# Optimization experiments

Measured on AMD Instinct MI355X. Metric: run time of the kernel, lower is better.

## Reference

```python
import jax, jax.numpy as jnp
import numpy as np

B, T, M, S, D, H, DH, P = 4, 1024, 1024, 1024, 1024, 16, 64, 4096


def layernorm(x, g, b, eps=1e-5):
    mu = x.mean(-1, keepdims=True)
    var = ((x - mu) ** 2).mean(-1, keepdims=True)
    return (x - mu) * jax.lax.rsqrt(var + eps) * g + b


def rel_shift(x):
    # Transformer-XL relative shift on [B,H,q,k] BD scores
    b, h, q, k = x.shape
    x = jnp.pad(x, ((0, 0), (0, 0), (0, 0), (1, 0)))
    return x.reshape(b, h, k + 1, q)[:, :, 1:, :].reshape(b, h, q, k)


def rel_attention(x, kv, mem, mask, pos_emb, r_w_bias, r_r_bias,
                  Wq, Wk, Wv, Wr, Wo, g, bln):
    # x: [B,Tq,D] queries; kv: [B,Skv,D]; mem: optional [B,M,D]
    cat = kv if mem is None else jnp.concatenate([mem, kv], axis=1)
    Bb, Tq, _ = x.shape
    K = cat.shape[1]
    q = (x @ Wq).reshape(Bb, Tq, H, DH)
    k = (cat @ Wk).reshape(Bb, K, H, DH)
    v = (cat @ Wv).reshape(Bb, K, H, DH)
    r = (pos_emb[-K:] @ Wr).reshape(K, H, DH)  # rel-pos keys, most-recent K positions
    AC = jnp.einsum('bthd,bkhd->bhtk', q + r_w_bias, k)
    BD = rel_shift(jnp.einsum('bthd,khd->bhtk', q + r_r_bias, r))
    scores = (AC + BD) * (1.0 / np.sqrt(DH))
    scores = jnp.where(mask[:, None, :, :], jnp.asarray(-1e30, scores.dtype), scores)
    prob = jax.nn.softmax(scores, axis=-1)
    o = jnp.einsum('bhtk,bkhd->bthd', prob, v).reshape(Bb, Tq, H * DH) @ Wo
    return layernorm(x + o, g, bln), cat, prob  # post-LN residual; cat is new memory


def residual_ff(x, W1, b1, W2, b2, g, bln):
    h = jax.nn.relu(x @ W1 + b1) @ W2 + b2
    return layernorm(x + h, g, bln)


def setup_inputs() -> dict:
    key = jax.random.key(0)
    ks = jax.random.split(key, 24)
    w = lambda i, shape: jax.random.normal(ks[i], shape, jnp.float32) * 0.02
    causal = jnp.triu(jnp.ones((T, M + T), bool), k=M + 1)  # True = masked
    return {
        'src': jax.random.normal(ks[0], (B, S, D), jnp.float32),
        'tgt': jax.random.normal(ks[1], (B, T, D), jnp.float32),
        'tgt_mem': jax.random.normal(ks[2], (B, M, D), jnp.float32),
        'pos_emb': w(3, (M + T, D)),
        'r_w_bias': w(4, (H, DH)),
        'r_r_bias': w(5, (H, DH)),
        'Wq1': w(6, (D, H * DH)), 'Wk1': w(7, (D, H * DH)), 'Wv1': w(8, (D, H * DH)),
        'Wr1': w(9, (D, H * DH)), 'Wo1': w(10, (H * DH, D)),
        'ln1_g': jnp.ones((D,), jnp.float32), 'ln1_b': jnp.zeros((D,), jnp.float32),
        'Wq2': w(11, (D, H * DH)), 'Wk2': w(12, (D, H * DH)), 'Wv2': w(13, (D, H * DH)),
        'Wr2': w(14, (D, H * DH)), 'Wo2': w(15, (H * DH, D)),
        'ln2_g': jnp.ones((D,), jnp.float32), 'ln2_b': jnp.zeros((D,), jnp.float32),
        'Wf1': w(16, (D, P)), 'bf1': jnp.zeros((P,), jnp.float32),
        'Wf2': w(17, (P, D)), 'bf2': jnp.zeros((D,), jnp.float32),
        'ln3_g': jnp.ones((D,), jnp.float32), 'ln3_b': jnp.zeros((D,), jnp.float32),
        'tgt_mask': jnp.broadcast_to(causal, (B, T, M + T)),
        'tgt_to_src_mask': jnp.zeros((B, T, S), bool),
    }


def reference(src, tgt, tgt_mem, pos_emb, r_w_bias, r_r_bias,
              Wq1, Wk1, Wv1, Wr1, Wo1, ln1_g, ln1_b,
              Wq2, Wk2, Wv2, Wr2, Wo2, ln2_g, ln2_b,
              Wf1, bf1, Wf2, bf2, ln3_g, ln3_b,
              tgt_mask, tgt_to_src_mask):
    out, new_mem, self_att_prob = rel_attention(
        tgt, tgt, tgt_mem, tgt_mask, pos_emb, r_w_bias, r_r_bias,
        Wq1, Wk1, Wv1, Wr1, Wo1, ln1_g, ln1_b)
    out, _, inter_att_prob = rel_attention(
        out, src, None, tgt_to_src_mask, pos_emb, r_w_bias, r_r_bias,
        Wq2, Wk2, Wv2, Wr2, Wo2, ln2_g, ln2_b)
    out = residual_ff(out, Wf1, bf1, Wf2, bf2, ln3_g, ln3_b)
    return (out, new_mem, self_att_prob, inter_att_prob)
```

## Files before the change

kernel.cpp:

```cpp
#include <hip/hip_runtime.h>

typedef unsigned short u16;
typedef __attribute__((ext_vector_type(8))) short short8;
typedef __attribute__((ext_vector_type(4))) float f4;
typedef __attribute__((ext_vector_type(4))) unsigned short u16x4;

__device__ __forceinline__ float b2f(u16 u) {
    unsigned int x = ((unsigned int)u) << 16;
    return __builtin_bit_cast(float, x);
}
__device__ __forceinline__ u16 f2b(float f) {
    unsigned int u = __builtin_bit_cast(unsigned int, f);
    u += 0x7FFFu + ((u >> 16) & 1u);
    return (u16)(u >> 16);
}

__device__ __forceinline__ void gl16(const void* g, void* l) {
    __builtin_amdgcn_global_load_lds(
        (const __attribute__((address_space(1))) void*)g,
        (__attribute__((address_space(3))) void*)l, 16, 0, 0);
}

template<int FM, int FN, int CBF, int EPI>
__global__ __launch_bounds__(256, 3)
void gemm_bt(const u16* __restrict__ Ap, const u16* __restrict__ Bp,
             void* __restrict__ Cp, const float* __restrict__ bias,
             int M, int N, int K, int lda, int ldb, int ldc,
             long long sAh, long long sAb, long long sBh, long long sBb,
             long long sCh, long long sCb, int batchH)
{
    constexpr int BM = FM * 32;
    constexpr int BN = FN * 32;
    __shared__ __align__(16) u16 As[2][BM * 32];
    __shared__ __align__(16) u16 Bs[2][BN * 32];

    const int tid  = threadIdx.x;
    const int z    = blockIdx.z;
    const int bb   = z / batchH;
    const int hh   = z - bb * batchH;
    const int m0   = blockIdx.y * BM;
    const int n0   = blockIdx.x * BN;
    const int w    = tid >> 6;
    const int lane = tid & 63;
    const int wr   = w >> 1;
    const int wc   = w & 1;
    const int lrow = lane & 15;
    const int lk   = (lane >> 4) << 3;
    const int lrow4 = lane >> 2;
    const int lch   = lane & 3;

    const u16* Ag = Ap + sAb * bb + sAh * hh;
    const u16* Bg = Bp + sBb * bb + sBh * hh;

    f4 acc[FM][FN] = {};

    auto stage = [&](int buf, int kt) {
        const int kb = kt << 5;
        #pragma unroll
        for (int i = 0; i < BM / 64; ++i) {
            const int row0 = (w + i * 4) << 4;
            gl16(Ag + (long long)(m0 + row0 + lrow4) * lda + kb + (lch << 3),
                 &As[buf][row0 * 32]);
        }
        #pragma unroll
        for (int i = 0; i < BN / 64; ++i) {
            const int row0 = (w + i * 4) << 4;
            gl16(Bg + (long long)(n0 + row0 + lrow4) * ldb + kb + (lch << 3),
                 &Bs[buf][row0 * 32]);
        }
    };

    const int nKt = K >> 5;
    stage(0, 0);
    __syncthreads();
    int cur = 0;
    for (int kt = 0; kt < nKt; ++kt) {
        if (kt + 1 < nKt) stage(cur ^ 1, kt + 1);

        short8 af[FM], bv[FN];
        #pragma unroll
        for (int m = 0; m < FM; ++m)
            af[m] = *(const short8*)(&As[cur][(wr * FM * 16 + m * 16 + lrow) * 32 + lk]);
        #pragma unroll
        for (int n = 0; n < FN; ++n)
            bv[n] = *(const short8*)(&Bs[cur][(wc * FN * 16 + n * 16 + lrow) * 32 + lk]);
        #pragma unroll
        for (int m = 0; m < FM; ++m)
            #pragma unroll
            for (int n = 0; n < FN; ++n)
                acc[m][n] = __builtin_amdgcn_mfma_f32_16x16x32_bf16(af[m], bv[n], acc[m][n], 0, 0, 0);

        __syncthreads();
        cur ^= 1;
    }

    const int crow0 = m0 + wr * FM * 16 + ((lane >> 4) << 2);
    const int ccol0 = n0 + wc * FN * 16 + lrow;
    if (CBF == 0) {
        float* Cg = (float*)Cp + sCb * bb + sCh * hh;
        #pragma unroll
        for (int m = 0; m < FM; ++m) {
            #pragma unroll
            for (int n = 0; n < FN; ++n) {
                const int col = ccol0 + n * 16;
                float bvv = (EPI >= 1) ? bias[col] : 0.f;
                #pragma unroll
                for (int r = 0; r < 4; ++r) {
                    float vv = acc[m][n][r] + bvv;
                    if (EPI == 2) vv = fmaxf(vv, 0.f);
                    Cg[(long long)(crow0 + m * 16 + r) * ldc + col] = vv;
                }
            }
        }
    } else {
        u16* Cg = (u16*)Cp + sCb * bb + sCh * hh;
        #pragma unroll
        for (int m = 0; m < FM; ++m) {
            #pragma unroll
            for (int n = 0; n < FN; ++n) {
                const int col = ccol0 + n * 16;
                float bvv = (EPI >= 1) ? bias[col] : 0.f;
                #pragma unroll
                for (int r = 0; r < 4; ++r) {
                    float vv = acc[m][n][r] + bvv;
                    if (EPI == 2) vv = fmaxf(vv, 0.f);
                    Cg[(long long)(crow0 + m * 16 + r) * ldc + col] = f2b(vv);
                }
            }
        }
    }
}

template<int KK, int MODE>
__global__ __launch_bounds__(512, 4)
void fattn(const u16* __restrict__ qsrc, long long qld, long long qsb,
           const float* __restrict__ rwb, const float* __restrict__ rrb,
           const u16* __restrict__ kb, const u16* __restrict__ rr,
           const u16* __restrict__ vt,
           float* __restrict__ probs, u16* __restrict__ ob, int kld)
{
    constexpr int LE = KK + 8;
    constexpr int NT = KK / 16;
    constexpr int NI = NT / 8;
    __shared__ __align__(16) u16 e[16 * LE];
    __shared__ __align__(16) u16 qws[16 * 72];
    __shared__ __align__(16) u16 qrs[17 * 72];
    __shared__ float psum[8][16];

    const int tid = threadIdx.x;
    const int bh  = blockIdx.y;
    const int b   = bh >> 4, h = bh & 15;
    const int t0  = blockIdx.x << 4;

    if (tid < 264) {
        int row, ch; const float* bias; u16* dst; bool act = true;
        if (tid < 128)      { row = tid >> 3;        ch = tid & 7; bias = rwb; dst = &qws[row * 72 + ch * 8]; }
        else if (tid < 256) { row = (tid - 128) >> 3; ch = tid & 7; bias = rrb; dst = &qrs[row * 72 + ch * 8]; }
        else if (MODE == 1) { row = 16;              ch = tid - 256; bias = rrb; dst = &qrs[16 * 72 + ch * 8]; }
        else act = false;
        if (act) {
            int trow = t0 + row; if (trow > 1023) trow = 1023;
            short8 qv = *(const short8*)(qsrc + b * qsb + (long long)trow * qld + h * 64 + ch * 8);
            const float* bp = bias + h * 64 + ch * 8;
            f4 b0 = *(const f4*)bp, b1 = *(const f4*)(bp + 4);
            short8 o;
            o[0] = (short)f2b((b2f((u16)qv[0]) + b0.x) * 0.125f);
            o[1] = (short)f2b((b2f((u16)qv[1]) + b0.y) * 0.125f);
            o[2] = (short)f2b((b2f((u16)qv[2]) + b0.z) * 0.125f);
            o[3] = (short)f2b((b2f((u16)qv[3]) + b0.w) * 0.125f);
            o[4] = (short)f2b((b2f((u16)qv[4]) + b1.x) * 0.125f);
            o[5] = (short)f2b((b2f((u16)qv[5]) + b1.y) * 0.125f);
            o[6] = (short)f2b((b2f((u16)qv[6]) + b1.z) * 0.125f);
            o[7] = (short)f2b((b2f((u16)qv[7]) + b1.w) * 0.125f);
            *(short8*)dst = o;
        }
    }
    __syncthreads();

    const int w = tid >> 6, lane = tid & 63;
    const int lc = lane & 15, g = lane >> 4, lk = g << 3;
    const int t = t0 + lc;

    const short8 bq0 = *(const short8*)&qws[lc * 72 + lk];
    const short8 bq1 = *(const short8*)&qws[lc * 72 + 32 + lk];
    const short8 br0 = *(const short8*)&qrs[lc * 72 + lk];
    const short8 br1 = *(const short8*)&qrs[lc * 72 + 32 + lk];
    short8 bs0 = {}, bs1 = {};
    if (MODE == 1) {
        bs0 = *(const short8*)&qrs[(lc + 1) * 72 + lk];
        bs1 = *(const short8*)&qrs[(lc + 1) * 72 + 32 + lk];
    }

    #pragma unroll
    for (int Bb = 0; Bb < NI; Bb += 2) {
        short8 R0[2], R1[2];
        #pragma unroll
        for (int u = 0; u < 2; ++u) {
            const int ut = w + (Bb + u) * 8;
            const int u0 = ut << 4;
            const bool nd = (u0 + t0 + 30 >= 1023) || (MODE == 1 && u0 + t0 <= 1021);
            if (nd) {
                const u16* rg = rr + (long long)(u0 + lc) * 2048 + h * 64;
                R0[u] = *(const short8*)(rg + lk);
                R1[u] = *(const short8*)(rg + 32 + lk);
            }
        }
        #pragma unroll
        for (int u = 0; u < 2; ++u) {
            const int ut = w + (Bb + u) * 8;
            const int u0 = ut << 4;
            const bool need1 = (u0 + t0 + 30 >= 1023);
            const bool need2 = (MODE == 1) && (u0 + t0 <= 1021);
            if (need1) {
                f4 acc = {};
                acc = __builtin_amdgcn_mfma_f32_16x16x32_bf16(R0[u], br0, acc, 0, 0, 0);
                acc = __builtin_amdgcn_mfma_f32_16x16x32_bf16(R1[u], br1, acc, 0, 0, 0);
                #pragma unroll
                for (int i = 0; i < 4; ++i) {
                    const int j = u0 + 4 * g + i + t - 1023;
                    if (j >= 0) e[lc * LE + j] = f2b(acc[i]);
                }
            }
            if (MODE == 1 && need2) {
                f4 acc = {};
                acc = __builtin_amdgcn_mfma_f32_16x16x32_bf16(R0[u], bs0, acc, 0, 0, 0);
                acc = __builtin_amdgcn_mfma_f32_16x16x32_bf16(R1[u], bs1, acc, 0, 0, 0);
                #pragma unroll
                for (int i = 0; i < 4; ++i) {
                    const int j = u0 + 4 * g + i + t + 2;
                    if (j < KK) e[lc * LE + j] = f2b(acc[i]);
                }
            }
        }
    }
    __syncthreads();

    float sum = 0.f;
    const int limit = t + 1024;
    const int jvt = (MODE == 0) ? ((t0 + 1039) >> 4) : (NT - 1);
    #pragma unroll
    for (int Bb = 0; Bb < NI; Bb += 4) {
        short8 K0[4], K1[4];
        #pragma unroll
        for (int u = 0; u < 4; ++u) {
            const int jt = w + (Bb + u) * 8;
            if (MODE != 0 || jt <= jvt) {
                const u16* kg = kb + (long long)(b * KK + (jt << 4) + lc) * kld + h * 64;
                K0[u] = *(const short8*)(kg + lk);
                K1[u] = *(const short8*)(kg + 32 + lk);
            }
        }
        #pragma unroll
        for (int u = 0; u < 4; ++u) {
            const int jt = w + (Bb + u) * 8;
            const int jme = (jt << 4) + 4 * g;
            if (MODE == 0 && jt > jvt) {
                u16x4 z = {0, 0, 0, 0};
                *(u16x4*)&e[lc * LE + jme] = z;
            } else {
                f4 acc = {};
                acc = __builtin_amdgcn_mfma_f32_16x16x32_bf16(K0[u], bq0, acc, 0, 0, 0);
                acc = __builtin_amdgcn_mfma_f32_16x16x32_bf16(K1[u], bq1, acc, 0, 0, 0);
                u16x4 bd4 = *(const u16x4*)&e[lc * LE + jme];
                u16x4 st;
                #pragma unroll
                for (int i = 0; i < 4; ++i) {
                    const int j = jme + i;
                    float bd = b2f(bd4[i]);
                    if (MODE == 1 && j == t + 1) bd = 0.f;
                    float ev = __expf(acc[i] + bd);
                    if (MODE == 0 && j > limit) ev = 0.f;
                    sum += ev;
                    st[i] = f2b(ev);
                }
                *(u16x4*)&e[lc * LE + jme] = st;
            }
        }
    }
    sum += __shfl_xor(sum, 16);
    sum += __shfl_xor(sum, 32);
    if (g == 0) psum[w][lc] = sum;
    __syncthreads();

    if (w >= 4) {
        const int r = (tid >> 4) & 15;
        const int q = tid & 15;
        float s = 0.f;
        #pragma unroll
        for (int w2 = 0; w2 < 8; ++w2) s += psum[w2][r];
        const float inv = 1.f / s;
        float* pr = probs + ((long long)bh * 1024 + t0 + r) * KK;
        #pragma unroll 4
        for (int i2 = 0; i2 < KK / 128; ++i2) {
            const int j0 = q * 8 + i2 * 128;
            u16x4 e0 = *(const u16x4*)&e[r * LE + j0];
            u16x4 e1 = *(const u16x4*)&e[r * LE + j0 + 4];
            f4 p0, p1;
            p0.x = b2f(e0.x) * inv; p0.y = b2f(e0.y) * inv;
            p0.z = b2f(e0.z) * inv; p0.w = b2f(e0.w) * inv;
            p1.x = b2f(e1.x) * inv; p1.y = b2f(e1.y) * inv;
            p1.z = b2f(e1.z) * inv; p1.w = b2f(e1.w) * inv;
            __builtin_nontemporal_store(p0, (f4*)(pr + j0));
            __builtin_nontemporal_store(p1, (f4*)(pr + j0 + 4));
        }
    } else {
        const int db = w << 4;
        const u16* vrow = vt + ((long long)(bh * 64 + db + lc)) * KK + lk;
        int kcend = KK / 32;
        if (MODE == 0) {
            const int ke = (t0 + 1071) >> 5;
            if (ke < kcend) kcend = ke;
        }
        f4 acc = {};
        #pragma unroll 2
        for (int kc = 0; kc < kcend; ++kc) {
            short8 a = *(const short8*)&e[lc * LE + kc * 32 + lk];
            short8 bv = *(const short8*)(vrow + kc * 32);
            acc = __builtin_amdgcn_mfma_f32_16x16x32_bf16(a, bv, acc, 0, 0, 0);
        }
        #pragma unroll
        for (int i = 0; i < 4; ++i) {
            const int trow = g * 4 + i;
            float s = 0.f;
            #pragma unroll
            for (int w2 = 0; w2 < 8; ++w2) s += psum[w2][trow];
            ob[((long long)(b * 1024 + t0 + trow)) * 1024 + h * 64 + db + lc] = f2b(acc[i] / s);
        }
    }
}

__global__ void conv_f2b(const float* __restrict__ in, u16* __restrict__ out, long long n4)
{
    long long i = (long long)blockIdx.x * 256 + threadIdx.x;
    if (i >= n4) return;
    f4 v = *(const f4*)(in + i * 4);
    u16x4 o; o.x = f2b(v.x); o.y = f2b(v.y); o.z = f2b(v.z); o.w = f2b(v.w);
    *(u16x4*)(out + i * 4) = o;
}

__global__ void concat_mem(const float* __restrict__ mem, const float* __restrict__ tgt,
                           float* __restrict__ nm, u16* __restrict__ cat)
{
    long long i = (long long)blockIdx.x * 256 + threadIdx.x;
    long long b = i >> 19;
    int rem = (int)(i & 524287);
    int r = rem >> 8, c4 = rem & 255;
    const float* sp = (r < 1024) ? (mem + ((b << 10) + r) * 1024 + c4 * 4)
                                 : (tgt + ((b << 10) + (r - 1024)) * 1024 + c4 * 4);
    f4 v = *(const f4*)sp;
    __builtin_nontemporal_store(v, (f4*)(nm + i * 4));
    u16x4 o; o.x = f2b(v.x); o.y = f2b(v.y); o.z = f2b(v.z); o.w = f2b(v.w);
    *(u16x4*)(cat + i * 4) = o;
}

struct TWS { const float* s; u16* d; int sld, dld; };
struct TW18 { TWS t[18]; };
__global__ void transpose_w18(TW18 p)
{
    __shared__ float tile[32][33];
    const TWS ts = p.t[blockIdx.z];
    int c0 = blockIdx.x * 32, r0 = blockIdx.y * 32;
    int tx = threadIdx.x, ty = threadIdx.y;
    tile[ty][tx] = ts.s[(long long)(r0 + ty) * ts.sld + c0 + tx];
    __syncthreads();
    ts.d[(long long)(c0 + ty) * ts.dld + r0 + tx] = f2b(tile[tx][ty]);
}

__global__ __launch_bounds__(256) void transpose_v(const u16* __restrict__ v, u16* __restrict__ vt,
                                                   int KK, int ld, int coff)
{
    __shared__ u16 tile[64][68];
    const int z = blockIdx.z, b = z >> 4, h = z & 15;
    const int j0 = blockIdx.x << 6;
    const int rr8 = threadIdx.x >> 3;
    const int c8 = (threadIdx.x & 7) << 3;
    #pragma unroll
    for (int p = 0; p < 2; ++p) {
        const int jr = p * 32 + rr8;
        short8 val = *(const short8*)(v + ((long long)(b * KK + j0 + jr)) * ld + coff + h * 64 + c8);
        #pragma unroll
        for (int k = 0; k < 8; ++k) tile[c8 + k][jr] = (u16)val[k];
    }
    __syncthreads();
    #pragma unroll
    for (int p = 0; p < 2; ++p) {
        const int d = p * 32 + rr8;
        short8 o;
        #pragma unroll
        for (int k = 0; k < 8; ++k) o[k] = (short)tile[d][c8 + k];
        *(short8*)(vt + ((long long)((b * 16 + h) * 64 + d)) * KK + j0 + c8) = o;
    }
}

__global__ __launch_bounds__(256) void ln_res(const float* __restrict__ x,
                                              const float* __restrict__ h1,
                                              const float* __restrict__ h2,
                                              const float* __restrict__ hbias,
                                              const float* __restrict__ g, const float* __restrict__ bl,
                                              float* __restrict__ o32, u16* __restrict__ obf)
{
    const long long row = blockIdx.x;
    const int tid = threadIdx.x;
    const long long base = row * 1024 + tid * 4;
    f4 xa = *(const f4*)(x + base);
    f4 ha = *(const f4*)(h1 + base);
    f4 hb = *(const f4*)(h2 + base);
    f4 hc = {0.f, 0.f, 0.f, 0.f};
    if (hbias) hc = *(const f4*)(hbias + tid * 4);
    float v0 = xa.x + ha.x + hb.x + hc.x, v1 = xa.y + ha.y + hb.y + hc.y;
    float v2 = xa.z + ha.z + hb.z + hc.z, v3 = xa.w + ha.w + hb.w + hc.w;
    float lsum = v0 + v1 + v2 + v3;
    float lsq = v0 * v0 + v1 * v1 + v2 * v2 + v3 * v3;
    #pragma unroll
    for (int o2 = 32; o2; o2 >>= 1) { lsum += __shfl_xor(lsum, o2); lsq += __shfl_xor(lsq, o2); }
    __shared__ float r1[4], r2[4];
    int w = tid >> 6, lane = tid & 63;
    if (lane == 0) { r1[w] = lsum; r2[w] = lsq; }
    __syncthreads();
    lsum = r1[0] + r1[1] + r1[2] + r1[3];
    lsq  = r2[0] + r2[1] + r2[2] + r2[3];
    const float mu = lsum * 0.0009765625f;
    const float var = lsq * 0.0009765625f - mu * mu;
    const float rsd = rsqrtf(var + 1e-5f);
    const int c = tid * 4;
    f4 gv = *(const f4*)(g + c);
    f4 bv = *(const f4*)(bl + c);
    f4 y;
    y.x = (v0 - mu) * rsd * gv.x + bv.x;
    y.y = (v1 - mu) * rsd * gv.y + bv.y;
    y.z = (v2 - mu) * rsd * gv.z + bv.z;
    y.w = (v3 - mu) * rsd * gv.w + bv.w;
    *(f4*)(o32 + base) = y;
    if (obf) {
        u16x4 u; u.x = f2b(y.x); u.y = f2b(y.y); u.z = f2b(y.z); u.w = f2b(y.w);
        *(u16x4*)(obf + base) = u;
    }
}

extern "C" void kernel_launch(void* const* d_in, const int* in_sizes, int n_in,
                              void* d_out, int out_size, void* d_ws, size_t ws_size,
                              hipStream_t stream)
{
    (void)in_sizes; (void)n_in; (void)out_size;
    const float* src  = (const float*)d_in[0];
    const float* tgt  = (const float*)d_in[1];
    const float* mem  = (const float*)d_in[2];
    const float* pos  = (const float*)d_in[3];
    const float* rwb  = (const float*)d_in[4];
    const float* rrb  = (const float*)d_in[5];
    const float* Wq1  = (const float*)d_in[6];
    const float* Wk1  = (const float*)d_in[7];
    const float* Wv1  = (const float*)d_in[8];
    const float* Wr1  = (const float*)d_in[9];
    const float* Wo1  = (const float*)d_in[10];
    const float* ln1g = (const float*)d_in[11];
    const float* ln1b = (const float*)d_in[12];
    const float* Wq2  = (const float*)d_in[13];
    const float* Wk2  = (const float*)d_in[14];
    const float* Wv2  = (const float*)d_in[15];
    const float* Wr2  = (const float*)d_in[16];
    const float* Wo2  = (const float*)d_in[17];
    const float* ln2g = (const float*)d_in[18];
    const float* ln2b = (const float*)d_in[19];
    const float* Wf1  = (const float*)d_in[20];
    const float* bf1  = (const float*)d_in[21];
    const float* Wf2  = (const float*)d_in[22];
    const float* bf2  = (const float*)d_in[23];
    const float* ln3g = (const float*)d_in[24];
    const float* ln3b = (const float*)d_in[25];

    float* outp   = (float*)d_out;
    float* newmem = outp + 4194304;
    float* selfP  = outp + 12582912;
    float* interP = outp + 146800640;

    char* ws = (char*)d_ws;
    size_t off = 0;
    auto alloc = [&](size_t bytes) -> void* {
        void* p = ws + off;
        off = (off + bytes + 255) & ~(size_t)255;
        return p;
    };
    u16*   src_bf  = (u16*)alloc(8u << 20);
    u16*   cat_bf  = (u16*)alloc(16u << 20);
    u16*   pos_bf  = (u16*)alloc(4u << 20);
    u16*   W1t    = (u16*)alloc(6u << 20);
    u16*   Wr12t  = (u16*)alloc(4u << 20);
    u16*   W2t    = (u16*)alloc(4u << 20);
    u16*   Wq2t   = (u16*)alloc(2u << 20);
    u16*   Wo1t   = (u16*)alloc(2u << 20);
    u16*   Wo2t   = (u16*)alloc(2u << 20);
    u16*   Wf1t   = (u16*)alloc(8u << 20);
    u16*   Wf2t   = (u16*)alloc(8u << 20);
    u16*   P1kv   = (u16*)alloc(34u << 20);
    u16*   qb1    = (u16*)alloc(8u << 20);
    u16*   P2k    = (u16*)alloc(8u << 20);
    u16*   P2v    = (u16*)alloc(8u << 20);
    u16*   R12    = (u16*)alloc(8u << 20);
    u16*   qb2    = (u16*)alloc(8u << 20);
    u16*   vtb    = (u16*)alloc(16u << 20);
    u16*   ob     = (u16*)alloc(8u << 20);
    float* projb  = (float*)alloc(16u << 20);
    float* projb2 = (float*)alloc(16u << 20);
    float* out1_32 = (float*)alloc(16u << 20);
    u16*   out1_bf = (u16*)alloc(8u << 20);
    float* out2_32 = (float*)alloc(16u << 20);
    u16*   out2_bf = (u16*)alloc(8u << 20);
    u16*   hb     = (u16*)alloc(32u << 20);
    if (off > ws_size) return;
    const long long PJ2 = projb2 - projb;

    dim3 tb(32, 32);

    concat_mem<<<8192, 256, 0, stream>>>(mem, tgt, newmem, cat_bf);
    conv_f2b<<<4096, 256, 0, stream>>>(src, src_bf, 1048576);
    conv_f2b<<<2048, 256, 0, stream>>>(pos, pos_bf, 524288);
    TW18 tw;
    tw.t[0] = {Wq1, W1t, 1024, 1024};
    tw.t[1] = {Wk1, W1t + 1048576, 1024, 1024};
    tw.t[2] = {Wv1, W1t + 2097152, 1024, 1024};
    tw.t[3] = {Wr1, Wr12t, 1024, 1024};
    tw.t[4] = {Wr2, Wr12t + 1048576, 1024, 1024};
    tw.t[5] = {Wk2, W2t, 1024, 1024};
    tw.t[6] = {Wv2, W2t + 1048576, 1024, 1024};
    tw.t[7] = {Wq2, Wq2t, 1024, 1024};
    tw.t[8] = {Wo1, Wo1t, 1024, 1024};
    tw.t[9] = {Wo2, Wo2t, 1024, 1024};
    for (int zz = 0; zz < 4; ++zz) {
        tw.t[10 + zz] = {Wf1 + zz * 1024, Wf1t + (long long)zz * 1048576, 4096, 1024};
        tw.t[14 + zz] = {Wf2 + (long long)zz * 1048576, Wf2t + zz * 1024, 1024, 4096};
    }
    transpose_w18<<<dim3(32, 32, 18), tb, 0, stream>>>(tw);

    gemm_bt<4,4,1,0><<<dim3(16,64,1), 256, 0, stream>>>(cat_bf, W1t + 1048576, P1kv, nullptr,
        8192,2048,1024, 1024,1024,2080, 0,0,0,0,0,0, 1);
    gemm_bt<4,4,1,0><<<dim3(8,8,4), 256, 0, stream>>>(cat_bf + 1048576, W1t, qb1, nullptr,
        1024,1024,1024, 1024,1024,1024, 0,2048LL*1024, 0,0, 0,1048576LL, 1);
    gemm_bt<4,4,1,0><<<dim3(16,16,1), 256, 0, stream>>>(pos_bf, Wr12t, R12, nullptr,
        2048,2048,1024, 1024,1024,2048, 0,0,0,0,0,0, 1);
    transpose_v<<<dim3(32,1,64), 256, 0, stream>>>(P1kv, vtb, 2048, 2080, 1024);
    fattn<2048,0><<<dim3(64,64), 512, 0, stream>>>(qb1, 1024LL, 1048576LL,
        rwb, rrb, P1kv, R12, vtb, selfP, ob, 2080);
    gemm_bt<4,4,0,0><<<dim3(8,32,2), 256, 0, stream>>>(ob, Wo1t, projb, nullptr,
        4096,1024,512, 1024,1024,1024, 0,512, 0,512, 0,PJ2, 1);
    ln_res<<<4096, 256, 0, stream>>>(tgt, projb, projb2, nullptr, ln1g, ln1b, out1_32, out1_bf);

    {
        const long long dA = (long long)(src_bf - out1_bf);
        const long long dB1 = (long long)(W2t - Wq2t);
        const long long dB2 = (long long)((W2t + 1048576) - Wq2t);
        const long long dC1 = (long long)(P2k - qb2);
        const long long dC2 = (long long)(P2v - qb2);
        gemm_bt<4,4,1,0><<<dim3(8,32,3), 256, 0, stream>>>(out1_bf, Wq2t, qb2, nullptr,
            4096,1024,1024, 1024,1024,1024, dA,dA, dB1,dB2, dC1,dC2, 2);
    }
    transpose_v<<<dim3(16,1,64), 256, 0, stream>>>(P2v, vtb, 1024, 1024, 0);
    fattn<1024,1><<<dim3(64,64), 512, 0, stream>>>(qb2, 1024LL, 1048576LL,
        rwb, rrb, P2k, R12 + 1024LL * 2048 + 1024, vtb, interP, ob, 1024);
    gemm_bt<4,4,0,0><<<dim3(8,32,2), 256, 0, stream>>>(ob, Wo2t, projb, nullptr,
        4096,1024,512, 1024,1024,1024, 0,512, 0,512, 0,PJ2, 1);
    ln_res<<<4096, 256, 0, stream>>>(out1_32, projb, projb2, nullptr, ln2g, ln2b, out2_32, out2_bf);

    gemm_bt<4,4,1,2><<<dim3(32,32,1), 256, 0, stream>>>(out2_bf, Wf1t, hb, bf1,
        4096,4096,1024, 1024,1024,4096, 0,0,0,0,0,0, 1);
    gemm_bt<4,4,0,0><<<dim3(8,32,2), 256, 0, stream>>>(hb, Wf2t, projb, nullptr,
        4096,1024,2048, 4096,4096,1024, 0,2048, 0,2048, 0,PJ2, 1);
    ln_res<<<4096, 256, 0, stream>>>(out2_32, projb, projb2, bf2, ln3g, ln3b, outp, nullptr);
}
```

Before: 928.3 us.

## Prefetch K tiles, remap attention blocks per XCD, set MFMA priority, fuse prep kernels

In the attention kernel, the first half of each K tile is now double-buffered so the next group's loads are issued before the current group's MFMA and exp work. The MFMA sections are also wrapped in s_setprio. The grid becomes 1-D with a block-id swizzle that groups consecutive query tiles of the same batch-head onto one XCD, aiming for better L2 reuse of K/V. Three small conversion kernels are merged into a single launch. The prefetch raises register pressure, which could hurt occupancy under launch_bounds(512,4).

```diff
diff --git a/kernel.cpp b/kernel.cpp
--- a/kernel.cpp
+++ b/kernel.cpp
@@ -142,15 +142,18 @@
     constexpr int LE = KK + 8;
     constexpr int NT = KK / 16;
     constexpr int NI = NT / 8;
+    constexpr int NB = NI / 4;
     __shared__ __align__(16) u16 e[16 * LE];
     __shared__ __align__(16) u16 qws[16 * 72];
     __shared__ __align__(16) u16 qrs[17 * 72];
     __shared__ float psum[8][16];
 
     const int tid = threadIdx.x;
-    const int bh  = blockIdx.y;
+    const int bid = blockIdx.x;
+    const int nid = ((bid & 7) << 9) + (bid >> 3);
+    const int bh  = nid >> 6;
+    const int t0  = (nid & 63) << 4;
     const int b   = bh >> 4, h = bh & 15;
-    const int t0  = blockIdx.x << 4;
 
     if (tid < 264) {
         int row, ch; const float* bias; u16* dst; bool act = true;
@@ -238,43 +241,60 @@
     float sum = 0.f;
     const int limit = t + 1024;
     const int jvt = (MODE == 0) ? ((t0 + 1039) >> 4) : (NT - 1);
-    #pragma unroll
-    for (int Bb = 0; Bb < NI; Bb += 4) {
-        short8 K0[4], K1[4];
-        #pragma unroll
-        for (int u = 0; u < 4; ++u) {
-            const int jt = w + (Bb + u) * 8;
-            if (MODE != 0 || jt <= jvt) {
-                const u16* kg = kb + (long long)(b * KK + (jt << 4) + lc) * kld + h * 64;
-                K0[u] = *(const short8*)(kg + lk);
-                K1[u] = *(const short8*)(kg + 32 + lk);
-            }
-        }
-        #pragma unroll
-        for (int u = 0; u < 4; ++u) {
-            const int jt = w + (Bb + u) * 8;
-            const int jme = (jt << 4) + 4 * g;
-            if (MODE == 0 && jt > jvt) {
-                u16x4 z = {0, 0, 0, 0};
-                *(u16x4*)&e[lc * LE + jme] = z;
-            } else {
-                f4 acc = {};
-                acc = __builtin_amdgcn_mfma_f32_16x16x32_bf16(K0[u], bq0, acc, 0, 0, 0);
-                acc = __builtin_amdgcn_mfma_f32_16x16x32_bf16(K1[u], bq1, acc, 0, 0, 0);
-                u16x4 bd4 = *(const u16x4*)&e[lc * LE + jme];
-                u16x4 st;
-                #pragma unroll
-                for (int i = 0; i < 4; ++i) {
-                    const int j = jme + i;
-                    float bd = b2f(bd4[i]);
-                    if (MODE == 1 && j == t + 1) bd = 0.f;
-                    float ev = __expf(acc[i] + bd);
-                    if (MODE == 0 && j > limit) ev = 0.f;
-                    sum += ev;
-                    st[i] = f2b(ev);
-                }
-                *(u16x4*)&e[lc * LE + jme] = st;
-            }
+    {
+        short8 K0a[4], K0b[4], K1c[4];
+        auto ldK0 = [&](short8* dst, int B2) {
+            #pragma unroll
+            for (int u = 0; u < 4; ++u) {
+                const int jt = w + (B2 * 4 + u) * 8;
+                if (MODE != 0 || jt <= jvt) {
+                    const u16* kg = kb + (long long)(b * KK + (jt << 4) + lc) * kld + h * 64;
+                    dst[u] = *(const short8*)(kg + lk);
+                }
+            }
+        };
+        ldK0(K0a, 0);
+        #pragma unroll
+        for (int B2 = 0; B2 < NB; ++B2) {
+            short8* K0c = (B2 & 1) ? K0b : K0a;
+            short8* K0n = (B2 & 1) ? K0a : K0b;
+            #pragma unroll
+            for (int u = 0; u < 4; ++u) {
+                const int jt = w + (B2 * 4 + u) * 8;
+                if (MODE != 0 || jt <= jvt) {
+                    const u16* kg = kb + (long long)(b * KK + (jt << 4) + lc) * kld + h * 64;
+                    K1c[u] = *(const short8*)(kg + 32 + lk);
+                }
+            }
+            if (B2 + 1 < NB) ldK0(K0n, B2 + 1);
+            __builtin_amdgcn_s_setprio(1);
+            #pragma unroll
+            for (int u = 0; u < 4; ++u) {
+                const int jt = w + (B2 * 4 + u) * 8;
+                const int jme = (jt << 4) + 4 * g;
+                if (MODE == 0 && jt > jvt) {
+                    u16x4 z = {0, 0, 0, 0};
+                    *(u16x4*)&e[lc * LE + jme] = z;
+                } else {
+                    f4 acc = {};
+                    acc = __builtin_amdgcn_mfma_f32_16x16x32_bf16(K0c[u], bq0, acc, 0, 0, 0);
+                    acc = __builtin_amdgcn_mfma_f32_16x16x32_bf16(K1c[u], bq1, acc, 0, 0, 0);
+                    u16x4 bd4 = *(const u16x4*)&e[lc * LE + jme];
+                    u16x4 st;
+                    #pragma unroll
+                    for (int i = 0; i < 4; ++i) {
+                        const int j = jme + i;
+                        float bd = b2f(bd4[i]);
+                        if (MODE == 1 && j == t + 1) bd = 0.f;
+                        float ev = __expf(acc[i] + bd);
+                        if (MODE == 0 && j > limit) ev = 0.f;
+                        sum += ev;
+                        st[i] = f2b(ev);
+                    }
+                    *(u16x4*)&e[lc * LE + jme] = st;
+                }
+            }
+            __builtin_amdgcn_s_setprio(0);
         }
     }
     sum += __shfl_xor(sum, 16);
@@ -312,12 +332,14 @@
             if (ke < kcend) kcend = ke;
         }
         f4 acc = {};
+        __builtin_amdgcn_s_setprio(1);
         #pragma unroll 2
         for (int kc = 0; kc < kcend; ++kc) {
             short8 a = *(const short8*)&e[lc * LE + kc * 32 + lk];
             short8 bv = *(const short8*)(vrow + kc * 32);
             acc = __builtin_amdgcn_mfma_f32_16x16x32_bf16(a, bv, acc, 0, 0, 0);
         }
+        __builtin_amdgcn_s_setprio(0);
         #pragma unroll
         for (int i = 0; i < 4; ++i) {
             const int trow = g * 4 + i;
@@ -329,28 +351,35 @@
     }
 }
 
-__global__ void conv_f2b(const float* __restrict__ in, u16* __restrict__ out, long long n4)
-{
-    long long i = (long long)blockIdx.x * 256 + threadIdx.x;
-    if (i >= n4) return;
-    f4 v = *(const f4*)(in + i * 4);
-    u16x4 o; o.x = f2b(v.x); o.y = f2b(v.y); o.z = f2b(v.z); o.w = f2b(v.w);
-    *(u16x4*)(out + i * 4) = o;
-}
-
-__global__ void concat_mem(const float* __restrict__ mem, const float* __restrict__ tgt,
-                           float* __restrict__ nm, u16* __restrict__ cat)
-{
-    long long i = (long long)blockIdx.x * 256 + threadIdx.x;
-    long long b = i >> 19;
-    int rem = (int)(i & 524287);
-    int r = rem >> 8, c4 = rem & 255;
-    const float* sp = (r < 1024) ? (mem + ((b << 10) + r) * 1024 + c4 * 4)
-                                 : (tgt + ((b << 10) + (r - 1024)) * 1024 + c4 * 4);
-    f4 v = *(const f4*)sp;
-    __builtin_nontemporal_store(v, (f4*)(nm + i * 4));
-    u16x4 o; o.x = f2b(v.x); o.y = f2b(v.y); o.z = f2b(v.z); o.w = f2b(v.w);
-    *(u16x4*)(cat + i * 4) = o;
+__global__ void prep0(const float* __restrict__ mem, const float* __restrict__ tgt,
+                      const float* __restrict__ src, const float* __restrict__ pos,
+                      float* __restrict__ nm, u16* __restrict__ cat,
+                      u16* __restrict__ srcb, u16* __restrict__ posb)
+{
+    const int bid = blockIdx.x;
+    const int tid = threadIdx.x;
+    if (bid < 8192) {
+        long long i = (long long)bid * 256 + tid;
+        long long b = i >> 19;
+        int rem = (int)(i & 524287);
+        int r = rem >> 8, c4 = rem & 255;
+        const float* sp = (r < 1024) ? (mem + ((b << 10) + r) * 1024 + c4 * 4)
+                                     : (tgt + ((b << 10) + (r - 1024)) * 1024 + c4 * 4);
+        f4 v = *(const f4*)sp;
+        __builtin_nontemporal_store(v, (f4*)(nm + i * 4));
+        u16x4 o; o.x = f2b(v.x); o.y = f2b(v.y); o.z = f2b(v.z); o.w = f2b(v.w);
+        *(u16x4*)(cat + i * 4) = o;
+    } else if (bid < 12288) {
+        long long i = (long long)(bid - 8192) * 256 + tid;
+        f4 v = *(const f4*)(src + i * 4);
+        u16x4 o; o.x = f2b(v.x); o.y = f2b(v.y); o.z = f2b(v.z); o.w = f2b(v.w);
+        *(u16x4*)(srcb + i * 4) = o;
+    } else {
+        long long i = (long long)(bid - 12288) * 256 + tid;
+        f4 v = *(const f4*)(pos + i * 4);
+        u16x4 o; o.x = f2b(v.x); o.y = f2b(v.y); o.z = f2b(v.z); o.w = f2b(v.w);
+        *(u16x4*)(posb + i * 4) = o;
+    }
 }
 
 struct TWS { const float* s; u16* d; int sld, dld; };
@@ -512,9 +541,7 @@
 
     dim3 tb(32, 32);
 
-    concat_mem<<<8192, 256, 0, stream>>>(mem, tgt, newmem, cat_bf);
-    conv_f2b<<<4096, 256, 0, stream>>>(src, src_bf, 1048576);
-    conv_f2b<<<2048, 256, 0, stream>>>(pos, pos_bf, 524288);
+    prep0<<<14336, 256, 0, stream>>>(mem, tgt, src, pos, newmem, cat_bf, src_bf, pos_bf);
     TW18 tw;
     tw.t[0] = {Wq1, W1t, 1024, 1024};
     tw.t[1] = {Wk1, W1t + 1048576, 1024, 1024};
@@ -539,7 +566,7 @@
     gemm_bt<4,4,1,0><<<dim3(16,16,1), 256, 0, stream>>>(pos_bf, Wr12t, R12, nullptr,
         2048,2048,1024, 1024,1024,2048, 0,0,0,0,0,0, 1);
     transpose_v<<<dim3(32,1,64), 256, 0, stream>>>(P1kv, vtb, 2048, 2080, 1024);
-    fattn<2048,0><<<dim3(64,64), 512, 0, stream>>>(qb1, 1024LL, 1048576LL,
+    fattn<2048,0><<<4096, 512, 0, stream>>>(qb1, 1024LL, 1048576LL,
         rwb, rrb, P1kv, R12, vtb, selfP, ob, 2080);
     gemm_bt<4,4,0,0><<<dim3(8,32,2), 256, 0, stream>>>(ob, Wo1t, projb, nullptr,
         4096,1024,512, 1024,1024,1024, 0,512, 0,512, 0,PJ2, 1);
@@ -555,7 +582,7 @@
             4096,1024,1024, 1024,1024,1024, dA,dA, dB1,dB2, dC1,dC2, 2);
     }
     transpose_v<<<dim3(16,1,64), 256, 0, stream>>>(P2v, vtb, 1024, 1024, 0);
-    fattn<1024,1><<<dim3(64,64), 512, 0, stream>>>(qb2, 1024LL, 1048576LL,
+    fattn<1024,1><<<4096, 512, 0, stream>>>(qb2, 1024LL, 1048576LL,
         rwb, rrb, P2k, R12 + 1024LL * 2048 + 1024, vtb, interP, ob, 1024);
     gemm_bt<4,4,0,0><<<dim3(8,32,2), 256, 0, stream>>>(ob, Wo2t, projb, nullptr,
         4096,1024,512, 1024,1024,1024, 0,512, 0,512, 0,PJ2, 1);
```

New measurement: 903.2 us. -2.7%, faster.
